# Performance work log

Measured on AMD Instinct MI355X. Metric: run time of the kernel, lower is better.

The kernel has to match this reference:

```python
import jax, jax.numpy as jnp
import numpy as np

T, K, N, G = 8192, 1024, 2048, 8  # total_rows, k, n, num_groups


def setup_inputs() -> dict:
    key = jax.random.key(0)
    kA, kB, kO = jax.random.split(key, 3)
    A = jax.random.normal(kA, (T, K), dtype=jnp.float32)
    B = jax.random.normal(kB, (G, K, N), dtype=jnp.float32) * 0.02
    # monotonically increasing end-offsets; last offset covers all rows
    offsets = jnp.sort(jax.random.randint(kO, (G,), 1, T)).at[-1].set(T).astype(jnp.int32)
    return {"A": A, "B": B, "offsets": offsets}


def reference(A, B, offsets):
    """Grouped GEMM: rows A[offsets[g-1]:offsets[g]] are multiplied by B[g].

    Implemented jit-compatibly (offsets may be traced) by masking rows per
    group and accumulating disjoint contributions; the Python loop is over
    the small, static number of groups only.
    """
    num_groups = B.shape[0]
    total_rows = A.shape[0]
    # group id of each row: first offset strictly greater than row index
    gid = jnp.searchsorted(offsets, jnp.arange(total_rows), side="right")  # [T]
    out = jnp.zeros((total_rows, B.shape[2]), dtype=A.dtype)
    for g in range(num_groups):
        mask = (gid == g)[:, None]                      # [T,1] disjoint masks
        out = out + jnp.where(mask, A, 0.0) @ B[g]      # [T,n]
    return out
```

## Files before the change

### kernel.cpp

```cpp
#include <hip/hip_runtime.h>
#include <hip/hip_bf16.h>

#define T_ROWS 8192
#define K_DIM  1024
#define N_DIM  2048
#define G_NUM  8
#define CONVA_BLOCKS 2048
#define CONVB_BLOCKS 4096

typedef __attribute__((ext_vector_type(8))) short short8;
typedef __attribute__((ext_vector_type(4))) float v4f;

__device__ __forceinline__ unsigned short f2bf(float x) {
  unsigned int u = __builtin_bit_cast(unsigned int, x);
  u += 0x7fffu + ((u >> 16) & 1u);
  return (unsigned short)(u >> 16);
}
__device__ __forceinline__ unsigned int pk2(float a, float b) {
  return (unsigned int)f2bf(a) | ((unsigned int)f2bf(b) << 16);
}
__device__ __forceinline__ void async_cp16(const void* gsrc, void* ldst) {
  __builtin_amdgcn_global_load_lds(
      (const __attribute__((address_space(1))) void*)gsrc,
      (__attribute__((address_space(3))) void*)ldst, 16, 0, 0);
}

__global__ __launch_bounds__(256) void conv_fused(const float* __restrict__ A,
                                                  const float* __restrict__ B,
                                                  unsigned short* __restrict__ Ab,
                                                  unsigned short* __restrict__ Bt) {
  __shared__ float tile[64][65];
  const int bid = blockIdx.x;
  const int t = threadIdx.x;
  const int q3 = bid / 3, r3 = bid - q3 * 3;

  if (r3 == 0) {
    size_t idx = (size_t)q3 * 256 + t;
    const float4* src = (const float4*)A + idx * 4;
    float4 v0 = src[0], v1 = src[1], v2 = src[2], v3 = src[3];
    uint4 o0, o1;
    o0.x = pk2(v0.x, v0.y); o0.y = pk2(v0.z, v0.w);
    o0.z = pk2(v1.x, v1.y); o0.w = pk2(v1.z, v1.w);
    o1.x = pk2(v2.x, v2.y); o1.y = pk2(v2.z, v2.w);
    o1.z = pk2(v3.x, v3.y); o1.w = pk2(v3.z, v3.w);
    ((uint4*)Ab)[idx * 2]     = o0;
    ((uint4*)Ab)[idx * 2 + 1] = o1;
    return;
  }
  const int bidx = 2 * q3 + (r3 - 1);
  const int nt = bidx & 31;
  const int kt = (bidx >> 5) & 15;
  const int g  = bidx >> 9;
  const int c4 = t & 15;
  const int r  = t >> 4;

  const float* src = B + ((size_t)g * K_DIM + (size_t)kt * 64) * N_DIM + (size_t)nt * 64;
#pragma unroll
  for (int i = 0; i < 4; ++i) {
    int k = r + i * 16;
    float4 v = *(const float4*)(src + (size_t)k * N_DIM + c4 * 4);
    tile[k][c4 * 4 + 0] = v.x; tile[k][c4 * 4 + 1] = v.y;
    tile[k][c4 * 4 + 2] = v.z; tile[k][c4 * 4 + 3] = v.w;
  }
  __syncthreads();
  unsigned short* dst = Bt + ((size_t)g * N_DIM + (size_t)nt * 64) * K_DIM + (size_t)kt * 64;
#pragma unroll
  for (int i = 0; i < 2; ++i) {
    int idx = t + i * 256;
    int n = idx >> 3;
    int seg = idx & 7;
    unsigned int u0 = pk2(tile[seg * 8 + 0][n], tile[seg * 8 + 1][n]);
    unsigned int u1 = pk2(tile[seg * 8 + 2][n], tile[seg * 8 + 3][n]);
    unsigned int u2 = pk2(tile[seg * 8 + 4][n], tile[seg * 8 + 5][n]);
    unsigned int u3 = pk2(tile[seg * 8 + 6][n], tile[seg * 8 + 7][n]);
    uint4 o; o.x = u0; o.y = u1; o.z = u2; o.w = u3;
    *(uint4*)(dst + (size_t)n * K_DIM + seg * 8) = o;
  }
}

__global__ __launch_bounds__(512) void gemm_kernel(const unsigned short* __restrict__ Ab,
                                                   const unsigned short* __restrict__ Btb,
                                                   const int* __restrict__ offs,
                                                   float* __restrict__ out) {
  __shared__ char lds[131072];
  const int t = threadIdx.x;

  const int b = blockIdx.x;
  const int xcd = b & 7;
  const int j = b >> 3;
  const int mslot = xcd * 5 + (j >> 3);
  const int n0 = (j & 7) * 256;

  int prev = 0, cum = 0, row0 = 0, row_end = 0, g = 0, found = 0;
#pragma unroll
  for (int gg = 0; gg < G_NUM; ++gg) {
    int e = offs[gg];
    int tiles = (e - prev + 255) >> 8;
    if (!found && mslot < cum + tiles) {
      found = 1; g = gg; row0 = prev + (mslot - cum) * 256; row_end = e;
    }
    cum += tiles;
    prev = e;
  }
  if (!found) return;

  const int lane = t & 63;
  const int wv = t >> 6;
  const int wm = wv & 1;
  const int wn = wv >> 1;

  const int rq = t >> 2;
  const int t4 = (t & 3) ^ ((rq ^ (rq >> 2)) & 3);
  int rA0 = row0 + rq;       if (rA0 > T_ROWS - 1) rA0 = T_ROWS - 1;
  int rA1 = row0 + 128 + rq; if (rA1 > T_ROWS - 1) rA1 = T_ROWS - 1;
  const unsigned short* aSrc0 = Ab + (size_t)rA0 * K_DIM + t4 * 8;
  const unsigned short* aSrc1 = Ab + (size_t)rA1 * K_DIM + t4 * 8;
  const unsigned short* bSrc0 = Btb + ((size_t)g * N_DIM + n0 + rq) * K_DIM + t4 * 8;
  const unsigned short* bSrc1 = Btb + ((size_t)g * N_DIM + n0 + 128 + rq) * K_DIM + t4 * 8;

  const int lr = lane & 15;
  const int phx = ((lane >> 4) ^ ((lr ^ (lr >> 2)) & 3)) << 4;
  const int arow = (wm * 128 + lr) * 64 + phx;
  const int brow = (wn * 64 + lr) * 64 + phx + 16384;

  v4f acc[8][4];
#pragma unroll
  for (int i = 0; i < 8; ++i)
#pragma unroll
    for (int j2 = 0; j2 < 4; ++j2)
#pragma unroll
      for (int r = 0; r < 4; ++r) acc[i][j2][r] = 0.0f;

#define ISSUE_T(TILE, S2)                                                  \
  do {                                                                     \
    char* base_ = (char*)lds + (S2) * 32768 + t * 16;                      \
    async_cp16(aSrc0 + (TILE) * 32, base_);                                \
    async_cp16(aSrc1 + (TILE) * 32, base_ + 8192);                         \
    async_cp16(bSrc0 + (TILE) * 32, base_ + 16384);                        \
    async_cp16(bSrc1 + (TILE) * 32, base_ + 24576);                        \
  } while (0)

#define PHASE_T(S, TILE, VM)                                               \
  do {                                                                     \
    asm volatile("s_waitcnt vmcnt(" #VM ")" ::: "memory");                 \
    __builtin_amdgcn_s_barrier();                                          \
    __builtin_amdgcn_sched_barrier(0);                                     \
    if ((TILE) >= 0) ISSUE_T(TILE, ((S) + 3) & 3);                         \
    short8 af_[8], bf_[4];                                                 \
    {                                                                      \
      const char* ab_ = (const char*)lds + (S) * 32768 + arow;             \
      const char* bb_ = (const char*)lds + (S) * 32768 + brow;             \
      _Pragma("unroll")                                                    \
      for (int mf = 0; mf < 8; ++mf) af_[mf] = *(const short8*)(ab_ + mf * 1024); \
      _Pragma("unroll")                                                    \
      for (int nf = 0; nf < 4; ++nf) bf_[nf] = *(const short8*)(bb_ + nf * 1024); \
    }                                                                      \
    __builtin_amdgcn_s_setprio(1);                                         \
    _Pragma("unroll")                                                      \
    for (int mf = 0; mf < 8; ++mf)                                         \
      _Pragma("unroll")                                                    \
      for (int nf = 0; nf < 4; ++nf)                                       \
        acc[mf][nf] = __builtin_amdgcn_mfma_f32_16x16x32_bf16(af_[mf], bf_[nf], acc[mf][nf], 0, 0, 0); \
    __builtin_amdgcn_s_setprio(0);                                         \
    __builtin_amdgcn_sched_barrier(0);                                     \
  } while (0)

  ISSUE_T(0, 0);
  ISSUE_T(1, 1);
  ISSUE_T(2, 2);

#pragma unroll 1
  for (int tb = 0; tb < 28; tb += 4) {
    PHASE_T(0, tb + 3, 8);
    PHASE_T(1, tb + 4, 8);
    PHASE_T(2, tb + 5, 8);
    PHASE_T(3, tb + 6, 8);
  }
  PHASE_T(0, 31, 8);
  PHASE_T(1, -1, 8);
  PHASE_T(2, -1, 4);
  PHASE_T(3, -1, 0);

#undef PHASE_T
#undef ISSUE_T

  const int colBase = n0 + wn * 64 + lr;
  const int rowBase = row0 + wm * 128 + ((lane >> 4) << 2);
#pragma unroll
  for (int mf = 0; mf < 8; ++mf) {
#pragma unroll
    for (int nf = 0; nf < 4; ++nf) {
      int c = colBase + nf * 16;
#pragma unroll
      for (int r = 0; r < 4; ++r) {
        int rr = rowBase + mf * 16 + r;
        if (rr < row_end) out[(size_t)rr * N_DIM + c] = acc[mf][nf][r];
      }
    }
  }
}

__global__ __launch_bounds__(256) void fallback_kernel(const float* __restrict__ A,
                                                       const float* __restrict__ B,
                                                       const int* __restrict__ offs,
                                                       float* __restrict__ out) {
  int r = blockIdx.y;
  int c = blockIdx.x * 256 + threadIdx.x;
  int g = 0;
#pragma unroll
  for (int i = 0; i < G_NUM; ++i) g += (offs[i] <= r);
  const float* a = A + (size_t)r * K_DIM;
  const float* b = B + (size_t)g * K_DIM * N_DIM + c;
  float s = 0.f;
  for (int k = 0; k < K_DIM; ++k) s += a[k] * b[(size_t)k * N_DIM];
  out[(size_t)r * N_DIM + c] = s;
}

extern "C" void kernel_launch(void* const* d_in, const int* in_sizes, int n_in,
                              void* d_out, int out_size, void* d_ws, size_t ws_size,
                              hipStream_t stream) {
  const float* A = (const float*)d_in[0];
  const float* B = (const float*)d_in[1];
  const int* offs = (const int*)d_in[2];
  float* out = (float*)d_out;

  size_t need = ((size_t)T_ROWS * K_DIM + (size_t)G_NUM * K_DIM * N_DIM) * 2;
  if (ws_size < need) {
    dim3 grid(N_DIM / 256, T_ROWS);
    fallback_kernel<<<grid, 256, 0, stream>>>(A, B, offs, out);
    return;
  }
  unsigned short* Ab = (unsigned short*)d_ws;
  unsigned short* Btb = Ab + (size_t)T_ROWS * K_DIM;

  conv_fused<<<CONVA_BLOCKS + CONVB_BLOCKS, 256, 0, stream>>>(A, B, Ab, Btb);
  gemm_kernel<<<8 * 5 * 8, 512, 0, stream>>>(Ab, Btb, offs, out);
}
```

Before: 207.0 us.

## Shrink GEMM tile to 128x128 with 256 threads and double buffering

Replaces the 256x256 tile GEMM (512 threads, 4-stage 128KB LDS pipeline) with 128x128 tiles on 256 threads, a 2-stage 32KB LDS double buffer and a full vmcnt(0) wait each step. The grid grows from 320 to 1152 blocks with 9 m-slots per XCD. Smaller tiles cut per-block LDS and waste on partial group tiles, and should allow several blocks per CU to raise occupancy. In exchange, operand reuse per load is lower, global traffic is higher, and the shallower prefetch may expose memory latency.

After: 200.6 us. 1.03x faster.

```diff
diff --git a/kernel.cpp b/kernel.cpp
--- a/kernel.cpp
+++ b/kernel.cpp
@@ -78,26 +78,26 @@
   }
 }
 
-__global__ __launch_bounds__(512) void gemm_kernel(const unsigned short* __restrict__ Ab,
+__global__ __launch_bounds__(256) void gemm_kernel(const unsigned short* __restrict__ Ab,
                                                    const unsigned short* __restrict__ Btb,
                                                    const int* __restrict__ offs,
                                                    float* __restrict__ out) {
-  __shared__ char lds[131072];
+  __shared__ char lds[32768];
   const int t = threadIdx.x;
 
   const int b = blockIdx.x;
   const int xcd = b & 7;
   const int j = b >> 3;
-  const int mslot = xcd * 5 + (j >> 3);
-  const int n0 = (j & 7) * 256;
+  const int mslot = xcd * 9 + (j >> 4);
+  const int n0 = (j & 15) * 128;
 
   int prev = 0, cum = 0, row0 = 0, row_end = 0, g = 0, found = 0;
 #pragma unroll
   for (int gg = 0; gg < G_NUM; ++gg) {
     int e = offs[gg];
-    int tiles = (e - prev + 255) >> 8;
+    int tiles = (e - prev + 127) >> 7;
     if (!found && mslot < cum + tiles) {
-      found = 1; g = gg; row0 = prev + (mslot - cum) * 256; row_end = e;
+      found = 1; g = gg; row0 = prev + (mslot - cum) * 128; row_end = e;
     }
     cum += tiles;
     prev = e;
@@ -111,90 +111,82 @@
 
   const int rq = t >> 2;
   const int t4 = (t & 3) ^ ((rq ^ (rq >> 2)) & 3);
-  int rA0 = row0 + rq;       if (rA0 > T_ROWS - 1) rA0 = T_ROWS - 1;
-  int rA1 = row0 + 128 + rq; if (rA1 > T_ROWS - 1) rA1 = T_ROWS - 1;
+  int rA0 = row0 + rq;      if (rA0 > T_ROWS - 1) rA0 = T_ROWS - 1;
+  int rA1 = row0 + 64 + rq; if (rA1 > T_ROWS - 1) rA1 = T_ROWS - 1;
   const unsigned short* aSrc0 = Ab + (size_t)rA0 * K_DIM + t4 * 8;
   const unsigned short* aSrc1 = Ab + (size_t)rA1 * K_DIM + t4 * 8;
   const unsigned short* bSrc0 = Btb + ((size_t)g * N_DIM + n0 + rq) * K_DIM + t4 * 8;
-  const unsigned short* bSrc1 = Btb + ((size_t)g * N_DIM + n0 + 128 + rq) * K_DIM + t4 * 8;
+  const unsigned short* bSrc1 = Btb + ((size_t)g * N_DIM + n0 + 64 + rq) * K_DIM + t4 * 8;
 
   const int lr = lane & 15;
-  const int phx = ((lane >> 4) ^ ((lr ^ (lr >> 2)) & 3)) << 4;
-  const int arow = (wm * 128 + lr) * 64 + phx;
-  const int brow = (wn * 64 + lr) * 64 + phx + 16384;
-
-  v4f acc[8][4];
-#pragma unroll
-  for (int i = 0; i < 8; ++i)
+  const int phx = (((lane >> 4) ^ ((lr ^ (lr >> 2)) & 3)) << 4);
+
+  v4f acc[4][4];
+#pragma unroll
+  for (int i = 0; i < 4; ++i)
 #pragma unroll
     for (int j2 = 0; j2 < 4; ++j2)
 #pragma unroll
       for (int r = 0; r < 4; ++r) acc[i][j2][r] = 0.0f;
 
-#define ISSUE_T(TILE, S2)                                                  \
+#define ISSUE_T(BUF, KOFF)                                                 \
   do {                                                                     \
-    char* base_ = (char*)lds + (S2) * 32768 + t * 16;                      \
-    async_cp16(aSrc0 + (TILE) * 32, base_);                                \
-    async_cp16(aSrc1 + (TILE) * 32, base_ + 8192);                         \
-    async_cp16(bSrc0 + (TILE) * 32, base_ + 16384);                        \
-    async_cp16(bSrc1 + (TILE) * 32, base_ + 24576);                        \
+    char* ad_ = (char*)lds + (BUF) * 8192 + t * 16;                        \
+    char* bd_ = (char*)lds + 16384 + (BUF) * 8192 + t * 16;                \
+    async_cp16(aSrc0 + (KOFF), ad_);                                       \
+    async_cp16(aSrc1 + (KOFF), ad_ + 4096);                                \
+    async_cp16(bSrc0 + (KOFF), bd_);                                       \
+    async_cp16(bSrc1 + (KOFF), bd_ + 4096);                                \
   } while (0)
 
-#define PHASE_T(S, TILE, VM)                                               \
+#define STEP_T(P, KNEXT)                                                   \
   do {                                                                     \
-    asm volatile("s_waitcnt vmcnt(" #VM ")" ::: "memory");                 \
+    asm volatile("s_waitcnt vmcnt(0)" ::: "memory");                       \
     __builtin_amdgcn_s_barrier();                                          \
     __builtin_amdgcn_sched_barrier(0);                                     \
-    if ((TILE) >= 0) ISSUE_T(TILE, ((S) + 3) & 3);                         \
-    short8 af_[8], bf_[4];                                                 \
+    if ((KNEXT) < K_DIM) ISSUE_T((P) ^ 1, KNEXT);                          \
+    short8 a_[4], b_[4];                                                   \
     {                                                                      \
-      const char* ab_ = (const char*)lds + (S) * 32768 + arow;             \
-      const char* bb_ = (const char*)lds + (S) * 32768 + brow;             \
+      const char* ab_ = (const char*)lds + (P) * 8192 + (wm * 64 + lr) * 64 + phx;          \
+      const char* bb_ = (const char*)lds + 16384 + (P) * 8192 + (wn * 64 + lr) * 64 + phx;  \
       _Pragma("unroll")                                                    \
-      for (int mf = 0; mf < 8; ++mf) af_[mf] = *(const short8*)(ab_ + mf * 1024); \
+      for (int im = 0; im < 4; ++im) a_[im] = *(const short8*)(ab_ + im * 1024); \
       _Pragma("unroll")                                                    \
-      for (int nf = 0; nf < 4; ++nf) bf_[nf] = *(const short8*)(bb_ + nf * 1024); \
+      for (int in = 0; in < 4; ++in) b_[in] = *(const short8*)(bb_ + in * 1024); \
     }                                                                      \
     __builtin_amdgcn_s_setprio(1);                                         \
     _Pragma("unroll")                                                      \
-    for (int mf = 0; mf < 8; ++mf)                                         \
+    for (int im = 0; im < 4; ++im)                                         \
       _Pragma("unroll")                                                    \
-      for (int nf = 0; nf < 4; ++nf)                                       \
-        acc[mf][nf] = __builtin_amdgcn_mfma_f32_16x16x32_bf16(af_[mf], bf_[nf], acc[mf][nf], 0, 0, 0); \
+      for (int in = 0; in < 4; ++in)                                       \
+        acc[im][in] = __builtin_amdgcn_mfma_f32_16x16x32_bf16(a_[im], b_[in], acc[im][in], 0, 0, 0); \
     __builtin_amdgcn_s_setprio(0);                                         \
     __builtin_amdgcn_sched_barrier(0);                                     \
   } while (0)
 
   ISSUE_T(0, 0);
-  ISSUE_T(1, 1);
-  ISSUE_T(2, 2);
 
 #pragma unroll 1
-  for (int tb = 0; tb < 28; tb += 4) {
-    PHASE_T(0, tb + 3, 8);
-    PHASE_T(1, tb + 4, 8);
-    PHASE_T(2, tb + 5, 8);
-    PHASE_T(3, tb + 6, 8);
-  }
-  PHASE_T(0, 31, 8);
-  PHASE_T(1, -1, 8);
-  PHASE_T(2, -1, 4);
-  PHASE_T(3, -1, 0);
-
-#undef PHASE_T
+  for (int s2 = 0; s2 < 16; ++s2) {
+    int k0 = s2 * 64;
+    STEP_T(0, k0 + 32);
+    STEP_T(1, k0 + 64);
+  }
+
+#undef STEP_T
 #undef ISSUE_T
 
   const int colBase = n0 + wn * 64 + lr;
-  const int rowBase = row0 + wm * 128 + ((lane >> 4) << 2);
-#pragma unroll
-  for (int mf = 0; mf < 8; ++mf) {
-#pragma unroll
-    for (int nf = 0; nf < 4; ++nf) {
-      int c = colBase + nf * 16;
+  const int rowBase = row0 + wm * 64 + ((lane >> 4) << 2);
+#pragma unroll
+  for (int im = 0; im < 4; ++im) {
+#pragma unroll
+    for (int in = 0; in < 4; ++in) {
+      int c = colBase + in * 16;
 #pragma unroll
       for (int r = 0; r < 4; ++r) {
-        int rr = rowBase + mf * 16 + r;
-        if (rr < row_end) out[(size_t)rr * N_DIM + c] = acc[mf][nf][r];
+        int rr = rowBase + im * 16 + r;
+        if (rr < row_end) out[(size_t)rr * N_DIM + c] = acc[im][in][r];
       }
     }
   }
@@ -234,5 +226,5 @@
   unsigned short* Btb = Ab + (size_t)T_ROWS * K_DIM;
 
   conv_fused<<<CONVA_BLOCKS + CONVB_BLOCKS, 256, 0, stream>>>(A, B, Ab, Btb);
-  gemm_kernel<<<8 * 5 * 8, 512, 0, stream>>>(Ab, Btb, offs, out);
-}
+  gemm_kernel<<<8 * 9 * 16, 256, 0, stream>>>(Ab, Btb, offs, out);
+}
```
